# Performance work log

Hardware: AMD Instinct MI355X
Metric: run time of the kernel (lower is better)

## Reference

```python
import jax, jax.numpy as jnp
import numpy as np

N = 32768          # total nodes
C = 384            # in/out channels == embed_dim
E = 384            # embed_dim
G = 12             # tetrahedral group size
H = 1              # effective_num_heads = num_heads // G
D = 32             # head_dim = (E // G) // H
P = D // 2         # RoPE rotation pairs
SD = 3             # spatial dims
NUM_GRAPHS = 64
AVG_NUM_NODES = float(N) / NUM_GRAPHS  # 512.0, passed as avg_num_nodes


def rope_apply(t, phase):
    # t: [N,G,H,D], phase: [N,G,H,P]; rotate consecutive (even,odd) pairs
    c, s = jnp.cos(phase), jnp.sin(phase)
    t2 = t.reshape(*t.shape[:-1], P, 2)
    x1, x2 = t2[..., 0], t2[..., 1]
    rot = jnp.stack([x1 * c - x2 * s, x1 * s + x2 * c], axis=-1)
    return rot.reshape(t.shape)


def setup_inputs() -> dict:
    key = jax.random.key(0)
    ks = jax.random.split(key, 8)
    x = jax.random.normal(ks[0], (N, C), jnp.float32)
    pos = jax.random.normal(ks[1], (N, SD), jnp.float32)
    batch = jnp.sort(jax.random.randint(ks[2], (N,), 0, NUM_GRAPHS)).astype(jnp.int32)
    sc = 1.0 / np.sqrt(C).astype(np.float32)
    Wq = jax.random.normal(ks[3], (C, E), jnp.float32) * sc
    Wv = jax.random.normal(ks[4], (C, E), jnp.float32) * sc
    Wo = jax.random.normal(ks[5], (E, C), jnp.float32) * (1.0 / np.sqrt(E).astype(np.float32))
    freqs = jax.random.normal(ks[6], (G, H, P, SD), jnp.float32)  # freq_sigma = 1.0
    return {
        'x': x, 'pos': pos, 'batch': batch,
        'Wq': Wq, 'bq': jnp.zeros((E,), jnp.float32),
        'Wv': Wv, 'bv': jnp.zeros((E,), jnp.float32),
        'Wo': Wo, 'bo': jnp.zeros((C,), jnp.float32),
        'freqs': freqs,
    }


def reference(x, pos, batch, Wq, bq, Wv, bv, Wo, bo, freqs):
    # projections -> [N, G, H, D]
    q = (x @ Wq + bq).reshape(N, G, H, D)
    v = (x @ Wv + bv).reshape(N, G, H, D)
    # RoPE phase from positions: [N, G, H, P]
    phase = jnp.einsum('ns,ghps->nghp', pos, freqs)
    q = rope_apply(q, phase)
    k = rope_apply(jnp.ones_like(q), phase)  # use_key=False -> k_raw = ones
    # linear attention: per-node outer product, then per-graph segment sum
    kv = jnp.einsum('nghd,nghe->nghde', k, v)              # [N,G,H,D,D]
    kv_kernel = jax.ops.segment_sum(kv, batch, num_segments=NUM_GRAPHS)
    kv_kernel = kv_kernel / AVG_NUM_NODES                  # mean_aggregation=False
    out = jnp.einsum('nghd,nghde->nghe', q, kv_kernel[batch])
    out = out.reshape(N, -1)
    return out @ Wo + bo
```

## Files before the change

### kernel.cpp

```cpp
#include <hip/hip_runtime.h>


#define N_NODES 32768
#define K_DIM   384
#define P_PAIR  16
#define NUM_GRAPHS 64

typedef unsigned short u16;
typedef __bf16 bf16x8 __attribute__((ext_vector_type(8)));
typedef float  f32x4  __attribute__((ext_vector_type(4)));
typedef float  f32x16 __attribute__((ext_vector_type(16)));
typedef __attribute__((address_space(3))) void       lds_void;
typedef const __attribute__((address_space(1))) void gbl_void;

__device__ __forceinline__ u16 f2bf(float f) {
    unsigned int i = __float_as_uint(f);
    unsigned int r = i + 0x7FFFu + ((i >> 16) & 1u);
    return (u16)(r >> 16);
}
__device__ __forceinline__ float bf2f(u16 u) {
    union { unsigned int i; float f; } x;
    x.i = ((unsigned int)u) << 16;
    return x.f;
}

__global__ void prep(const float* __restrict__ x,
                     const float* __restrict__ Wq, const float* __restrict__ Wv,
                     const float* __restrict__ Wo,
                     u16* __restrict__ xb, u16* __restrict__ WqvT,
                     u16* __restrict__ WoT) {
    int b = blockIdx.x;
    if (b < 6144) {
        int i = (b * 256 + threadIdx.x) * 8;
        float4 a0 = *reinterpret_cast<const float4*>(x + i);
        float4 a1 = *reinterpret_cast<const float4*>(x + i + 4);
        union { u16 u[8]; float4 v; } pk;
        pk.u[0] = f2bf(a0.x); pk.u[1] = f2bf(a0.y);
        pk.u[2] = f2bf(a0.z); pk.u[3] = f2bf(a0.w);
        pk.u[4] = f2bf(a1.x); pk.u[5] = f2bf(a1.y);
        pk.u[6] = f2bf(a1.z); pk.u[7] = f2bf(a1.w);
        *reinterpret_cast<float4*>(xb + i) = pk.v;
    } else {
        int idx = (b - 6144) * 256 + threadIdx.x;
        if (idx < 294912) {
            int n = idx / 384, k = idx % 384;
            WqvT[idx] = f2bf(n < 384 ? Wq[k * 384 + n] : Wv[k * 384 + (n - 384)]);
        } else {
            int j = idx - 294912;
            int n = j / 384, k = j % 384;
            WoT[j] = f2bf(Wo[k * 384 + n]);
        }
    }
}

#define GEMM_CORE(A_PTR, B_PTR)                                                  \
    __shared__ __align__(1024) u16 T[8192];                                      \
    const int tid = threadIdx.x;                                                 \
    const int w = tid >> 6, lane = tid & 63;                                     \
    const int wr = (w >> 1) << 6, wc = (w & 1) << 6;                             \
    const int lm = lane & 15, q = lane >> 4;                                     \
    const int srow = lane >> 2, sc8 = (lane & 3) << 3;                           \
    f32x4 acc[4][4];                                                             \
    _Pragma("unroll") for (int i = 0; i < 4; i++)                                \
    _Pragma("unroll") for (int j = 0; j < 4; j++)                                \
    _Pragma("unroll") for (int r = 0; r < 4; r++) acc[i][j][r] = 0.0f;           \
    for (int k0 = 0; k0 < K_DIM; k0 += 32) {                                     \
        __syncthreads();                                                         \
        _Pragma("unroll")                                                        \
        for (int s = w; s < 16; s += 4) {                                        \
            int row = ((s & 7) << 4) + srow;                                     \
            const u16* gp = ((s >> 3) ? (B_PTR) + (size_t)(n0 + row) * K_DIM     \
                                      : (A_PTR) + (size_t)(m0 + row) * K_DIM)    \
                            + k0 + sc8;                                          \
            __builtin_amdgcn_global_load_lds((gbl_void*)gp,                      \
                                             (lds_void*)&T[s << 9], 16, 0, 0);   \
        }                                                                        \
        __syncthreads();                                                         \
        bf16x8 af[4], bfr[4];                                                    \
        _Pragma("unroll") for (int i = 0; i < 4; i++) {                          \
            af[i]  = *reinterpret_cast<const bf16x8*>(&T[(wr + i * 16 + lm) * 32 + q * 8]);          \
            bfr[i] = *reinterpret_cast<const bf16x8*>(&T[4096 + (wc + i * 16 + lm) * 32 + q * 8]);   \
        }                                                                        \
        _Pragma("unroll") for (int i = 0; i < 4; i++)                            \
        _Pragma("unroll") for (int j = 0; j < 4; j++)                            \
            acc[i][j] = __builtin_amdgcn_mfma_f32_16x16x32_bf16(af[i], bfr[j], acc[i][j], 0, 0, 0);  \
    }

__global__ __launch_bounds__(256) void gemm_qv(
    const u16* __restrict__ A, const u16* __restrict__ Bt,
    const float* __restrict__ bq, const float* __restrict__ bv,
    u16* __restrict__ Qw, u16* __restrict__ Vd) {
    const int b = blockIdx.x;
    const int xcd = b & 7, jj = b >> 3;
    const int by = xcd * 32 + jj / 6, bx = jj % 6;
    const int m0 = by << 7, n0 = bx << 7;
    GEMM_CORE(A, Bt)
    u16* Cq = (n0 < 384) ? Qw : Vd;
    const float* bias = (n0 < 384) ? bq : bv;
    const int coff = (n0 < 384) ? 0 : 384;
#pragma unroll
    for (int j = 0; j < 4; j++) {
        int gc = n0 + wc + j * 16 + lm - coff;
        float bs = bias[gc];
#pragma unroll
        for (int i = 0; i < 4; i++) {
            int gr = m0 + wr + i * 16 + q * 4;
#pragma unroll
            for (int r = 0; r < 4; r++)
                Cq[(size_t)(gr + r) * 384 + gc] = f2bf(acc[i][j][r] + bs);
        }
    }
}

__global__ __launch_bounds__(256) void gemm_out(
    const u16* __restrict__ A, const u16* __restrict__ Bt,
    const float* __restrict__ bias, float* __restrict__ Cmat) {
    const int b = blockIdx.x;
    const int xcd = b & 7, jj = b >> 3;
    const int by = xcd * 32 + jj / 3, bx = jj % 3;
    const int m0 = by << 7, n0 = bx << 7;
    GEMM_CORE(A, Bt)
#pragma unroll
    for (int j = 0; j < 4; j++) {
        int gc = n0 + wc + j * 16 + lm;
        float bs = bias[gc];
#pragma unroll
        for (int i = 0; i < 4; i++) {
            int gr = m0 + wr + i * 16 + q * 4;
#pragma unroll
            for (int r = 0; r < 4; r++)
                Cmat[(size_t)(gr + r) * 384 + gc] = acc[i][j][r] + bs;
        }
    }
}

__global__ __launch_bounds__(256) void kv_mfma(
    const u16* __restrict__ V, const float* __restrict__ pos,
    const int* __restrict__ batch, const float* __restrict__ freqs,
    float* __restrict__ KV) {
    const int bid = blockIdx.x;
    const int xcd = bid & 7, jj = bid >> 3;
    const int g = (xcd << 3) + jj / 12, grp = jj % 12;

    const int tid = threadIdx.x;
    const int w = tid >> 6, lane = tid & 63;
    const int hi = lane >> 5, de = lane & 31;
    const int p = de >> 1, sgn = de & 1;

    const float f0 = freqs[(grp * P_PAIR + p) * 3 + 0];
    const float f1 = freqs[(grp * P_PAIR + p) * 3 + 1];
    const float f2 = freqs[(grp * P_PAIR + p) * 3 + 2];

    int s0 = 0, s1 = N_NODES;
    while (s0 < s1) { int m = (s0 + s1) >> 1; if (batch[m] < g) s0 = m + 1; else s1 = m; }
    const int start = s0;
    int e0 = start, e1 = N_NODES;
    while (e0 < e1) { int m = (e0 + e1) >> 1; if (batch[m] < g + 1) e0 = m + 1; else e1 = m; }
    const int end = e0;

    __shared__ __align__(1024) u16 vbuf[2048];
    __shared__ float posb[192];
    __shared__ __align__(16) float red[4096];

    f32x16 acc;
#pragma unroll
    for (int r = 0; r < 16; r++) acc[r] = 0.0f;

    const int nl0 = w * 16 + hi * 8;

    for (int c = start; c < end; c += 64) {
        __syncthreads();
        if (tid < 192) {
            int i = c * 3 + tid;
            posb[tid] = (i < 3 * N_NODES) ? pos[i] : 0.0f;
        }
        {
            int r = tid >> 2;
            int nn = c + r;
            const u16* gp = V + (size_t)nn * K_DIM + (grp << 5) + ((tid & 3) << 3);
            if (nn < N_NODES)
                __builtin_amdgcn_global_load_lds((gbl_void*)gp,
                                                 (lds_void*)&vbuf[w << 9], 16, 0, 0);
        }
        __syncthreads();

        union { bf16x8 v; u16 u[8]; } A, B;
#pragma unroll
        for (int j = 0; j < 8; j++) {
            int nl = nl0 + j;
            int n = c + nl;
            float ph = posb[nl * 3 + 0] * f0 + posb[nl * 3 + 1] * f1
                     + posb[nl * 3 + 2] * f2;
            float sn, cs;
            __sincosf(ph, &sn, &cs);
            float kd = sgn ? (sn + cs) : (cs - sn);
            bool valid = n < end;
            A.u[j] = valid ? f2bf(kd) : (u16)0;
            B.u[j] = valid ? vbuf[(nl << 5) + de] : (u16)0;
        }
        acc = __builtin_amdgcn_mfma_f32_32x32x16_bf16(A.v, B.v, acc, 0, 0, 0);
    }

#pragma unroll
    for (int r = 0; r < 16; r++) {
        int d = (r & 3) + ((r >> 2) << 3) + (hi << 2);
        red[(w << 10) + (d << 5) + de] = acc[r];
    }
    __syncthreads();
    {
        int i4 = tid << 2;
        f32x4 a0 = *reinterpret_cast<const f32x4*>(&red[i4]);
        f32x4 a1 = *reinterpret_cast<const f32x4*>(&red[1024 + i4]);
        f32x4 a2 = *reinterpret_cast<const f32x4*>(&red[2048 + i4]);
        f32x4 a3 = *reinterpret_cast<const f32x4*>(&red[3072 + i4]);
        f32x4 s = (a0 + a1 + a2 + a3) * (1.0f / 512.0f);
        *reinterpret_cast<f32x4*>(&KV[((size_t)(g * 12 + grp) << 10) + i4]) = s;
    }
}

__global__ __launch_bounds__(384) void attn_k(
    u16* __restrict__ Qw, const float* __restrict__ pos,
    const int* __restrict__ batch, const float* __restrict__ freqs,
    const float* __restrict__ KV) {
    const int nb = blockIdx.x << 6;
    const int t = threadIdx.x;
    const int grp = t >> 5, ec = t & 31;
    const int p = ec >> 1, sgn = ec & 1;
    const float f0 = freqs[(grp * P_PAIR + p) * 3 + 0];
    const float f1 = freqs[(grp * P_PAIR + p) * 3 + 1];
    const float f2 = freqs[(grp * P_PAIR + p) * 3 + 2];

    __shared__ float qbuf[8][384];
    __shared__ int gbuf[8];
    float kv[32];
    int gcur = -1;
    const int cq = t & ~1;

    for (int base = nb; base < nb + 64; base += 8) {
        __syncthreads();
        if (t < 8) gbuf[t] = batch[base + t];
#pragma unroll
        for (int i = 0; i < 8; i++) {
            int n = base + i;
            float qa = bf2f(Qw[(size_t)n * 384 + cq]);
            float qb = bf2f(Qw[(size_t)n * 384 + cq + 1]);
            float ph = pos[n * 3 + 0] * f0 + pos[n * 3 + 1] * f1 + pos[n * 3 + 2] * f2;
            float sn, cs;
            __sincosf(ph, &sn, &cs);
            qbuf[i][t] = sgn ? (qa * sn + qb * cs) : (qa * cs - qb * sn);
        }
        __syncthreads();
#pragma unroll
        for (int i = 0; i < 8; i++) {
            int g = gbuf[i];
            if (g != gcur) {
                gcur = g;
                const float* src = KV + ((g * 12 + grp) << 10) + ec;
#pragma unroll
                for (int d = 0; d < 32; d++) kv[d] = src[d << 5];
            }
            const float* qr = &qbuf[i][grp << 5];
            float o = 0.0f;
#pragma unroll
            for (int d = 0; d < 32; d++) o = fmaf(qr[d], kv[d], o);
            Qw[(size_t)(base + i) * 384 + t] = f2bf(o);
        }
    }
}

extern "C" void kernel_launch(void* const* d_in, const int* in_sizes, int n_in,
                              void* d_out, int out_size, void* d_ws, size_t ws_size,
                              hipStream_t stream) {
    const float* x     = (const float*)d_in[0];
    const float* pos   = (const float*)d_in[1];
    const int*   batch = (const int*)d_in[2];
    const float* Wq    = (const float*)d_in[3];
    const float* bq    = (const float*)d_in[4];
    const float* Wv    = (const float*)d_in[5];
    const float* bv    = (const float*)d_in[6];
    const float* Wo    = (const float*)d_in[7];
    const float* bo    = (const float*)d_in[8];
    const float* fr    = (const float*)d_in[9];
    float* out = (float*)d_out;

    char* ws = (char*)d_ws;
    float* KV   = (float*)(ws);
    u16*   WqvT = (u16*)(ws + 3145728);
    u16*   WoT  = (u16*)(ws + 3735552);
    u16*   Qw   = (u16*)(ws + 4030464);
    u16*   Vd   = (u16*)d_out;
    u16*   xb   = (u16*)d_out + N_NODES * 384;

    prep<<<dim3(7872), dim3(256), 0, stream>>>(x, Wq, Wv, Wo, xb, WqvT, WoT);
    gemm_qv<<<dim3(1536), dim3(256), 0, stream>>>(xb, WqvT, bq, bv, Qw, Vd);
    kv_mfma<<<dim3(768), dim3(256), 0, stream>>>(Vd, pos, batch, fr, KV);
    attn_k<<<dim3(512), dim3(384), 0, stream>>>(Qw, pos, batch, fr, KV);
    gemm_out<<<dim3(768), dim3(256), 0, stream>>>(Qw, WoT, bo, out);
}
```

Before: 219.2 us.

## Replace scalar attention-apply kernel with MFMA bf16 per-group matmul

Rewrites the q·KV application step as a bf16 MFMA 32x32x16 kernel. Each block handles 128 nodes for one of the 12 groups. Block indices are arranged across XCDs, and graph boundaries inside a 32-node wave tile are handled by masking q rows and looping over the graphs present. This removes the per-thread scalar 32-term FMA loops and strided KV register loads. In exchange KV is rounded to bf16, which adds precision error. Launch width rises from 512 blocks of 384 threads to 3072 blocks of 256 threads.

```diff
diff --git a/kernel.cpp b/kernel.cpp
--- a/kernel.cpp
+++ b/kernel.cpp
@@ -218,53 +218,92 @@
     }
 }
 
-__global__ __launch_bounds__(384) void attn_k(
+__global__ __launch_bounds__(256) void attn_mfma(
     u16* __restrict__ Qw, const float* __restrict__ pos,
     const int* __restrict__ batch, const float* __restrict__ freqs,
     const float* __restrict__ KV) {
-    const int nb = blockIdx.x << 6;
-    const int t = threadIdx.x;
-    const int grp = t >> 5, ec = t & 31;
-    const int p = ec >> 1, sgn = ec & 1;
-    const float f0 = freqs[(grp * P_PAIR + p) * 3 + 0];
-    const float f1 = freqs[(grp * P_PAIR + p) * 3 + 1];
-    const float f2 = freqs[(grp * P_PAIR + p) * 3 + 2];
-
-    __shared__ float qbuf[8][384];
-    __shared__ int gbuf[8];
-    float kv[32];
-    int gcur = -1;
-    const int cq = t & ~1;
-
-    for (int base = nb; base < nb + 64; base += 8) {
-        __syncthreads();
-        if (t < 8) gbuf[t] = batch[base + t];
-#pragma unroll
-        for (int i = 0; i < 8; i++) {
-            int n = base + i;
-            float qa = bf2f(Qw[(size_t)n * 384 + cq]);
-            float qb = bf2f(Qw[(size_t)n * 384 + cq + 1]);
-            float ph = pos[n * 3 + 0] * f0 + pos[n * 3 + 1] * f1 + pos[n * 3 + 2] * f2;
-            float sn, cs;
-            __sincosf(ph, &sn, &cs);
-            qbuf[i][t] = sgn ? (qa * sn + qb * cs) : (qa * cs - qb * sn);
-        }
-        __syncthreads();
-#pragma unroll
-        for (int i = 0; i < 8; i++) {
-            int g = gbuf[i];
-            if (g != gcur) {
-                gcur = g;
-                const float* src = KV + ((g * 12 + grp) << 10) + ec;
-#pragma unroll
-                for (int d = 0; d < 32; d++) kv[d] = src[d << 5];
-            }
-            const float* qr = &qbuf[i][grp << 5];
-            float o = 0.0f;
-#pragma unroll
-            for (int d = 0; d < 32; d++) o = fmaf(qr[d], kv[d], o);
-            Qw[(size_t)(base + i) * 384 + t] = f2bf(o);
-        }
+    const int bid = blockIdx.x;
+    const int xcd = bid & 7, jj = bid >> 3;
+    const int chunk = (xcd << 5) + jj / 12, grp = jj % 12;
+    const int nbase = chunk << 7;
+
+    const int tid = threadIdx.x;
+    const int w = tid >> 6, lane = tid & 63;
+    const int hi = lane >> 5, de = lane & 31;
+
+    __shared__ float sfreq[48];
+    __shared__ __align__(16) float red[4096];
+
+    if (tid < 48) sfreq[tid] = freqs[grp * 48 + tid];
+
+    const int node = nbase + (w << 5) + de;
+    const float p0 = pos[node * 3 + 0];
+    const float p1 = pos[node * 3 + 1];
+    const float p2 = pos[node * 3 + 2];
+    const int bnode = batch[node];
+    const int g0 = batch[nbase + (w << 5)];
+    const int g1 = batch[nbase + (w << 5) + 31];
+
+    union { bf16x8 v; u16 u[8]; } qlo, qhi, alo, ahi;
+    {
+        const u16* qp = Qw + (size_t)node * K_DIM + (grp << 5) + (hi << 3);
+        qlo.v = *reinterpret_cast<const bf16x8*>(qp);
+        qhi.v = *reinterpret_cast<const bf16x8*>(qp + 16);
+    }
+    __syncthreads();
+#pragma unroll
+    for (int z = 0; z < 4; z++) {
+        const int pl = (hi << 2) + z;
+        const float* F  = &sfreq[pl * 3];
+        const float* F2 = &sfreq[(8 + pl) * 3];
+        float sn, cs, sn2, cs2;
+        __sincosf(p0 * F[0]  + p1 * F[1]  + p2 * F[2],  &sn,  &cs);
+        __sincosf(p0 * F2[0] + p1 * F2[1] + p2 * F2[2], &sn2, &cs2);
+        float x1 = bf2f(qlo.u[2 * z]), x2 = bf2f(qlo.u[2 * z + 1]);
+        alo.u[2 * z]     = f2bf(x1 * cs - x2 * sn);
+        alo.u[2 * z + 1] = f2bf(x1 * sn + x2 * cs);
+        float y1 = bf2f(qhi.u[2 * z]), y2 = bf2f(qhi.u[2 * z + 1]);
+        ahi.u[2 * z]     = f2bf(y1 * cs2 - y2 * sn2);
+        ahi.u[2 * z + 1] = f2bf(y1 * sn2 + y2 * cs2);
+    }
+
+    f32x16 oacc;
+#pragma unroll
+    for (int r = 0; r < 16; r++) oacc[r] = 0.0f;
+    for (int g = g0; g <= g1; g++) {
+        const bool msk = (bnode == g);
+        union { bf16x8 v; u16 u[8]; } ml, mh, bl, bh;
+#pragma unroll
+        for (int j = 0; j < 8; j++) {
+            ml.u[j] = msk ? alo.u[j] : (u16)0;
+            mh.u[j] = msk ? ahi.u[j] : (u16)0;
+        }
+        const float* kvp = KV + (((size_t)(g * 12 + grp)) << 10) + de;
+#pragma unroll
+        for (int j = 0; j < 8; j++) {
+            bl.u[j] = f2bf(kvp[(hi * 8 + j) << 5]);
+            bh.u[j] = f2bf(kvp[(16 + hi * 8 + j) << 5]);
+        }
+        oacc = __builtin_amdgcn_mfma_f32_32x32x16_bf16(ml.v, bl.v, oacc, 0, 0, 0);
+        oacc = __builtin_amdgcn_mfma_f32_32x32x16_bf16(mh.v, bh.v, oacc, 0, 0, 0);
+    }
+
+#pragma unroll
+    for (int r = 0; r < 16; r++) {
+        int rl = (r & 3) + ((r >> 2) << 3) + (hi << 2);
+        red[((w << 5) + rl) * 32 + de] = oacc[r];
+    }
+    __syncthreads();
+    {
+        const int row = tid >> 1, half = tid & 1;
+        union { u16 u[16]; float4 v[2]; } pk;
+#pragma unroll
+        for (int z = 0; z < 16; z++)
+            pk.u[z] = f2bf(red[row * 32 + half * 16 + z]);
+        float4* dst = reinterpret_cast<float4*>(
+            Qw + (size_t)(nbase + row) * K_DIM + (grp << 5) + (half << 4));
+        dst[0] = pk.v[0];
+        dst[1] = pk.v[1];
     }
 }
 
@@ -294,6 +333,6 @@
     prep<<<dim3(7872), dim3(256), 0, stream>>>(x, Wq, Wv, Wo, xb, WqvT, WoT);
     gemm_qv<<<dim3(1536), dim3(256), 0, stream>>>(xb, WqvT, bq, bv, Qw, Vd);
     kv_mfma<<<dim3(768), dim3(256), 0, stream>>>(Vd, pos, batch, fr, KV);
-    attn_k<<<dim3(512), dim3(384), 0, stream>>>(Qw, pos, batch, fr, KV);
+    attn_mfma<<<dim3(3072), dim3(256), 0, stream>>>(Qw, pos, batch, fr, KV);
     gemm_out<<<dim3(768), dim3(256), 0, stream>>>(Qw, WoT, bo, out);
 }
```

Result: faster. 202.9 us (-7.5%).
